# Performance work log

Measured on AMD Instinct MI355X. Metric: run time of the kernel, lower is better.

## Reference

```python
import jax, jax.numpy as jnp
import numpy as np

HEADS, OUT_C = 8, 16
NEG_SLOPE = 0.2  # PyG GATConv default negative_slope


def setup_inputs() -> dict:
    key = jax.random.key(0)
    ks = jax.random.split(key, 6)
    N, E, IN = 100000, 1600000, 128
    x = jax.random.normal(ks[0], (N, IN), jnp.float32)
    edge_index = jax.random.randint(ks[1], (2, E), 0, N, dtype=jnp.int32)
    W = jax.random.normal(ks[2], (IN, HEADS * OUT_C), jnp.float32) / np.float32(np.sqrt(IN))
    att_src = jax.random.normal(ks[3], (HEADS, OUT_C), jnp.float32) * 0.1
    att_dst = jax.random.normal(ks[4], (HEADS, OUT_C), jnp.float32) * 0.1
    bias = jax.random.normal(ks[5], (HEADS * OUT_C,), jnp.float32) * 0.01
    return {"x": x, "edge_index": edge_index, "W": W,
            "att_src": att_src, "att_dst": att_dst, "bias": bias}


def reference(x, edge_index, W, att_src, att_dst, bias):
    N = x.shape[0]
    # Linear projection, split into heads: [N, H, C]
    xw = (x @ W).reshape(N, HEADS, OUT_C)
    # Add self-loops (PyG default add_self_loops=True)
    loops = jnp.arange(N, dtype=edge_index.dtype)
    src = jnp.concatenate([edge_index[0], loops])
    dst = jnp.concatenate([edge_index[1], loops])
    # Per-node attention terms [N, H], then per-edge logits
    a_s = jnp.einsum('nhc,hc->nh', xw, att_src)
    a_d = jnp.einsum('nhc,hc->nh', xw, att_dst)
    e = a_s[src] + a_d[dst]                       # [Etot, H]
    e = jnp.where(e > 0, e, NEG_SLOPE * e)        # LeakyReLU
    # Segment softmax over edges grouped by destination node
    emax = jax.ops.segment_max(e, dst, num_segments=N)
    p = jnp.exp(e - emax[dst])
    denom = jax.ops.segment_sum(p, dst, num_segments=N)
    alpha = p / (denom[dst] + 1e-16)              # [Etot, H]
    # Weighted scatter-aggregate of source messages
    out = jax.ops.segment_sum(xw[src] * alpha[:, :, None], dst, num_segments=N)
    out = out.reshape(N, HEADS * OUT_C) + bias    # concat heads + bias
    return jax.nn.relu(out)                       # act='relu', norm=None
```

## Files before the change

kernel.cpp:

```cpp
#include <hip/hip_runtime.h>
#include <math.h>

#define HEADS 8
#define OUTC 16
#define HC 128
#define NEG_SLOPE 0.2f

#define BM 128
#define BK 32
#define XPAD 132
#define CAP 64
#define CHUNK 2048

typedef unsigned int uint;
typedef unsigned short ushort;

__device__ __forceinline__ ushort f2bf(float f) {
    uint u = __float_as_uint(f);
    u += 0x7FFFu + ((u >> 16) & 1u);
    return (ushort)(u >> 16);
}

__global__ __launch_bounds__(256, 4) void k_fused(
    const float* __restrict__ x, const float* __restrict__ W,
    const float* __restrict__ att_src, const float* __restrict__ att_dst,
    const int* __restrict__ ei,
    ushort* __restrict__ xwh, float* __restrict__ a_s, float* __restrict__ a_d,
    int* __restrict__ deg, int* __restrict__ csr,
    int N, int E, int SBLK) {
    __shared__ float xs[BK][XPAD];
    __shared__ float Ws[BK][XPAD];

    if (blockIdx.x < SBLK) {
        int b = blockIdx.x;
        int chunk = b >> 3;
        int r = b & 7;
        int R8 = (N + 7) >> 3;
        int lo = r * R8;
        int hi = lo + R8; if (hi > N) hi = N;

        int cbase = chunk * CHUNK;
        int srcs[8], dsts[8];
#pragma unroll
        for (int g = 0; g < 2; ++g) {
            int e = cbase + g * 1024 + 4 * (int)threadIdx.x;
            if (e + 3 < E) {
                int4 s4 = *(const int4*)&ei[e];
                int4 d4 = *(const int4*)&ei[E + e];
                srcs[4 * g + 0] = s4.x; srcs[4 * g + 1] = s4.y;
                srcs[4 * g + 2] = s4.z; srcs[4 * g + 3] = s4.w;
                dsts[4 * g + 0] = d4.x; dsts[4 * g + 1] = d4.y;
                dsts[4 * g + 2] = d4.z; dsts[4 * g + 3] = d4.w;
            } else {
#pragma unroll
                for (int j = 0; j < 4; ++j) {
                    int ee = e + j;
                    if (ee < E) {
                        srcs[4 * g + j] = ei[ee];
                        dsts[4 * g + j] = ei[E + ee];
                    } else {
                        dsts[4 * g + j] = -1;
                    }
                }
            }
        }
#pragma unroll
        for (int k = 0; k < 8; ++k) {
            int d = dsts[k];
            if (d >= lo && d < hi) {
                int slot = atomicAdd(&deg[d], 1);
                if (slot < CAP) csr[(size_t)d * CAP + slot] = srcs[k];
            }
        }
        return;
    }

    int t = threadIdx.x;
    int nb0 = (blockIdx.x - SBLK) * BM;
    int tc = t & 15;
    int tr = t >> 4;

    float acc[8][8];
#pragma unroll
    for (int i = 0; i < 8; ++i)
#pragma unroll
        for (int j = 0; j < 8; ++j) acc[i][j] = 0.0f;

    for (int k0 = 0; k0 < HC; k0 += BK) {
        int kk4 = (t & 7) * 4;
#pragma unroll
        for (int p = 0; p < 4; ++p) {
            int nr = (t >> 3) + p * 32;
            int node = nb0 + nr;
            float4 v = make_float4(0.f, 0.f, 0.f, 0.f);
            if (node < N) v = *(const float4*)&x[(size_t)node * HC + k0 + kk4];
            xs[kk4 + 0][nr] = v.x;
            xs[kk4 + 1][nr] = v.y;
            xs[kk4 + 2][nr] = v.z;
            xs[kk4 + 3][nr] = v.w;
        }
        int kk = t >> 3;
        int c4 = (t & 7) * 4;
#pragma unroll
        for (int j = 0; j < 4; ++j) {
            *(float4*)&Ws[kk][c4 + j * 32] =
                *(const float4*)&W[(size_t)(k0 + kk) * HC + c4 + j * 32];
        }
        __syncthreads();

#pragma unroll 4
        for (int k = 0; k < BK; ++k) {
            float xa[8], wa[8];
            *(float4*)&xa[0] = *(const float4*)&xs[k][tr * 8];
            *(float4*)&xa[4] = *(const float4*)&xs[k][tr * 8 + 4];
            *(float4*)&wa[0] = *(const float4*)&Ws[k][tc * 8];
            *(float4*)&wa[4] = *(const float4*)&Ws[k][tc * 8 + 4];
#pragma unroll
            for (int i = 0; i < 8; ++i)
#pragma unroll
                for (int j = 0; j < 8; ++j)
                    acc[i][j] = fmaf(xa[i], wa[j], acc[i][j]);
        }
        __syncthreads();
    }

    float as8[8], ad8[8];
#pragma unroll
    for (int j = 0; j < 8; ++j) {
        as8[j] = att_src[tc * 8 + j];
        ad8[j] = att_dst[tc * 8 + j];
    }
    int h = tc >> 1;
#pragma unroll
    for (int i = 0; i < 8; ++i) {
        int node = nb0 + tr * 8 + i;
        float vs = 0.f, vd = 0.f;
        ushort h8[8];
#pragma unroll
        for (int j = 0; j < 8; ++j) {
            vs = fmaf(acc[i][j], as8[j], vs);
            vd = fmaf(acc[i][j], ad8[j], vd);
            h8[j] = f2bf(acc[i][j]);
        }
        vs += __shfl_xor(vs, 1);
        vd += __shfl_xor(vd, 1);
        if (node < N) {
            *(uint4*)&xwh[(size_t)node * HC + tc * 8] = *(uint4*)&h8[0];
            if ((tc & 1) == 0) {
                a_s[node * HEADS + h] = vs;
                a_d[node * HEADS + h] = vd;
            }
        }
    }
}

__global__ __launch_bounds__(256) void k_node(
    const int* __restrict__ deg, const int* __restrict__ csr,
    const float* __restrict__ a_s, const float* __restrict__ a_d,
    const uint* __restrict__ xwh, const float* __restrict__ bias,
    float* __restrict__ out, int N) {
    int n = blockIdx.x * 4 + (threadIdx.x >> 6);
    if (n >= N) return;
    int l = threadIdx.x & 63;
    int hB = l >> 3;

    float asn = a_s[n * HEADS + hB];
    float adn = a_d[n * HEADS + hB];

    float v = asn + adn;
    v = v > 0.0f ? v : NEG_SLOPE * v;
    float p = __expf(v);
    float den = p;
    uint w = xwh[n * 64 + l];
    float acc0 = p * __uint_as_float(w << 16);
    float acc1 = p * __uint_as_float(w & 0xFFFF0000u);

    int cnt = deg[n];
    if (cnt > CAP) cnt = CAP;
    const int* row = csr + (size_t)n * CAP;
#pragma unroll 4
    for (int i = 0; i < cnt; ++i) {
        int s = row[i];
        float vv = a_s[s * HEADS + hB] + adn;
        vv = vv > 0.0f ? vv : NEG_SLOPE * vv;
        float pp = __expf(vv);
        den += pp;
        uint ww = xwh[s * 64 + l];
        acc0 = fmaf(pp, __uint_as_float(ww << 16), acc0);
        acc1 = fmaf(pp, __uint_as_float(ww & 0xFFFF0000u), acc1);
    }

    float inv = 1.0f / (den + 1e-16f);
    float2 b = *(const float2*)&bias[2 * l];
    float r0 = acc0 * inv + b.x;
    float r1 = acc1 * inv + b.y;
    float2 o;
    o.x = r0 > 0.0f ? r0 : 0.0f;
    o.y = r1 > 0.0f ? r1 : 0.0f;
    *(float2*)&out[(size_t)n * HC + 2 * l] = o;
}

extern "C" void kernel_launch(void* const* d_in, const int* in_sizes, int n_in,
                              void* d_out, int out_size, void* d_ws, size_t ws_size,
                              hipStream_t stream) {
    const float* x       = (const float*)d_in[0];
    const int*   ei      = (const int*)d_in[1];
    const float* W       = (const float*)d_in[2];
    const float* att_src = (const float*)d_in[3];
    const float* att_dst = (const float*)d_in[4];
    const float* bias    = (const float*)d_in[5];
    float* out = (float*)d_out;

    int N = in_sizes[0] / HC;
    int E = in_sizes[1] / 2;

    ushort* xwh = (ushort*)d_ws;
    float* a_s  = (float*)(xwh + (size_t)N * HC);
    float* a_d  = a_s + (size_t)N * HEADS;
    int* deg    = (int*)(a_d + (size_t)N * HEADS);
    int* csr    = deg + N;

    hipMemsetAsync(deg, 0, (size_t)N * sizeof(int), stream);

    int GB = (N + BM - 1) / BM;
    int SC = (E + CHUNK - 1) / CHUNK;
    int SBLK = SC * 8;
    k_fused<<<SBLK + GB, 256, 0, stream>>>(x, W, att_src, att_dst, ei,
                                           xwh, a_s, a_d, deg, csr, N, E, SBLK);

    k_node<<<(N + 3) / 4, 256, 0, stream>>>(deg, csr, a_s, a_d,
                                            (const uint*)xwh, bias, out, N);
}
```

Measured before the change: 310.8 us.

## Batch neighbor gathers, use exp2 with prescaled logits, reorder blocks, halve BK

```diff
diff --git a/kernel.cpp b/kernel.cpp
--- a/kernel.cpp
+++ b/kernel.cpp
@@ -5,15 +5,19 @@
 #define OUTC 16
 #define HC 128
 #define NEG_SLOPE 0.2f
+#define LOG2E 1.44269504f
 
 #define BM 128
-#define BK 32
+#define BK 16
 #define XPAD 132
 #define CAP 64
 #define CHUNK 2048
 
 typedef unsigned int uint;
 typedef unsigned short ushort;
+typedef float  __attribute__((ext_vector_type(4))) f32x4;
+typedef int    __attribute__((ext_vector_type(4))) i32x4;
+typedef uint   __attribute__((ext_vector_type(4))) u32x4;
 
 __device__ __forceinline__ ushort f2bf(float f) {
     uint u = __float_as_uint(f);
@@ -27,26 +31,28 @@
     const int* __restrict__ ei,
     ushort* __restrict__ xwh, float* __restrict__ a_s, float* __restrict__ a_d,
     int* __restrict__ deg, int* __restrict__ csr,
-    int N, int E, int SBLK) {
+    int N, int E, int GB) {
     __shared__ float xs[BK][XPAD];
     __shared__ float Ws[BK][XPAD];
 
-    if (blockIdx.x < SBLK) {
-        int b = blockIdx.x;
-        int chunk = b >> 3;
-        int r = b & 7;
+    int bid = blockIdx.x;
+    if (bid >= GB) {
+        int i = bid - GB;
+        int chunk = i >> 3;
+        int r = bid & 7;
         int R8 = (N + 7) >> 3;
         int lo = r * R8;
         int hi = lo + R8; if (hi > N) hi = N;
 
         int cbase = chunk * CHUNK;
+        int t = threadIdx.x;
         int srcs[8], dsts[8];
 #pragma unroll
         for (int g = 0; g < 2; ++g) {
-            int e = cbase + g * 1024 + 4 * (int)threadIdx.x;
+            int e = cbase + g * 1024 + 4 * t;
             if (e + 3 < E) {
-                int4 s4 = *(const int4*)&ei[e];
-                int4 d4 = *(const int4*)&ei[E + e];
+                i32x4 s4 = __builtin_nontemporal_load((const i32x4*)&ei[e]);
+                i32x4 d4 = __builtin_nontemporal_load((const i32x4*)&ei[E + e]);
                 srcs[4 * g + 0] = s4.x; srcs[4 * g + 1] = s4.y;
                 srcs[4 * g + 2] = s4.z; srcs[4 * g + 3] = s4.w;
                 dsts[4 * g + 0] = d4.x; dsts[4 * g + 1] = d4.y;
@@ -76,7 +82,7 @@
     }
 
     int t = threadIdx.x;
-    int nb0 = (blockIdx.x - SBLK) * BM;
+    int nb0 = bid * BM;
     int tc = t & 15;
     int tr = t >> 4;
 
@@ -86,25 +92,28 @@
 #pragma unroll
         for (int j = 0; j < 8; ++j) acc[i][j] = 0.0f;
 
+    int kk4 = (t & 3) * 4;
+    int xr  = t >> 2;
+    int wk  = t >> 4;
+    int wc4 = (t & 15) * 4;
+
     for (int k0 = 0; k0 < HC; k0 += BK) {
-        int kk4 = (t & 7) * 4;
-#pragma unroll
-        for (int p = 0; p < 4; ++p) {
-            int nr = (t >> 3) + p * 32;
+#pragma unroll
+        for (int p = 0; p < 2; ++p) {
+            int nr = xr + p * 64;
             int node = nb0 + nr;
-            float4 v = make_float4(0.f, 0.f, 0.f, 0.f);
-            if (node < N) v = *(const float4*)&x[(size_t)node * HC + k0 + kk4];
+            f32x4 v = {0.f, 0.f, 0.f, 0.f};
+            if (node < N)
+                v = __builtin_nontemporal_load((const f32x4*)&x[(size_t)node * HC + k0 + kk4]);
             xs[kk4 + 0][nr] = v.x;
             xs[kk4 + 1][nr] = v.y;
             xs[kk4 + 2][nr] = v.z;
             xs[kk4 + 3][nr] = v.w;
         }
-        int kk = t >> 3;
-        int c4 = (t & 7) * 4;
-#pragma unroll
-        for (int j = 0; j < 4; ++j) {
-            *(float4*)&Ws[kk][c4 + j * 32] =
-                *(const float4*)&W[(size_t)(k0 + kk) * HC + c4 + j * 32];
+#pragma unroll
+        for (int j = 0; j < 2; ++j) {
+            *(float4*)&Ws[wk][wc4 + j * 64] =
+                *(const float4*)&W[(size_t)(k0 + wk) * HC + wc4 + j * 64];
         }
         __syncthreads();
 
@@ -145,10 +154,11 @@
         vs += __shfl_xor(vs, 1);
         vd += __shfl_xor(vd, 1);
         if (node < N) {
-            *(uint4*)&xwh[(size_t)node * HC + tc * 8] = *(uint4*)&h8[0];
+            u32x4 hv = *(u32x4*)&h8[0];
+            __builtin_nontemporal_store(hv, (u32x4*)&xwh[(size_t)node * HC + tc * 8]);
             if ((tc & 1) == 0) {
-                a_s[node * HEADS + h] = vs;
-                a_d[node * HEADS + h] = vd;
+                a_s[node * HEADS + h] = vs * LOG2E;
+                a_d[node * HEADS + h] = vd * LOG2E;
             }
         }
     }
@@ -164,12 +174,11 @@
     int l = threadIdx.x & 63;
     int hB = l >> 3;
 
-    float asn = a_s[n * HEADS + hB];
     float adn = a_d[n * HEADS + hB];
 
-    float v = asn + adn;
+    float v = a_s[n * HEADS + hB] + adn;
     v = v > 0.0f ? v : NEG_SLOPE * v;
-    float p = __expf(v);
+    float p = exp2f(v);
     float den = p;
     uint w = xwh[n * 64 + l];
     float acc0 = p * __uint_as_float(w << 16);
@@ -178,16 +187,34 @@
     int cnt = deg[n];
     if (cnt > CAP) cnt = CAP;
     const int* row = csr + (size_t)n * CAP;
-#pragma unroll 4
-    for (int i = 0; i < cnt; ++i) {
-        int s = row[i];
-        float vv = a_s[s * HEADS + hB] + adn;
-        vv = vv > 0.0f ? vv : NEG_SLOPE * vv;
-        float pp = __expf(vv);
-        den += pp;
-        uint ww = xwh[s * 64 + l];
-        acc0 = fmaf(pp, __uint_as_float(ww << 16), acc0);
-        acc1 = fmaf(pp, __uint_as_float(ww & 0xFFFF0000u), acc1);
+
+    for (int base = 0; base < cnt; base += 8) {
+        int sv[8];
+#pragma unroll
+        for (int j = 0; j < 8; ++j) {
+            int i = base + j;
+            sv[j] = (i < cnt) ? row[i] : -1;
+        }
+        float as8[8];
+        uint w8[8];
+#pragma unroll
+        for (int j = 0; j < 8; ++j) {
+            if (sv[j] >= 0) {
+                as8[j] = a_s[sv[j] * HEADS + hB];
+                w8[j]  = xwh[(size_t)sv[j] * 64 + l];
+            }
+        }
+#pragma unroll
+        for (int j = 0; j < 8; ++j) {
+            if (sv[j] >= 0) {
+                float vv = as8[j] + adn;
+                vv = vv > 0.0f ? vv : NEG_SLOPE * vv;
+                float pp = exp2f(vv);
+                den += pp;
+                acc0 = fmaf(pp, __uint_as_float(w8[j] << 16), acc0);
+                acc1 = fmaf(pp, __uint_as_float(w8[j] & 0xFFFF0000u), acc1);
+            }
+        }
     }
 
     float inv = 1.0f / (den + 1e-16f);
@@ -225,8 +252,8 @@
     int GB = (N + BM - 1) / BM;
     int SC = (E + CHUNK - 1) / CHUNK;
     int SBLK = SC * 8;
-    k_fused<<<SBLK + GB, 256, 0, stream>>>(x, W, att_src, att_dst, ei,
-                                           xwh, a_s, a_d, deg, csr, N, E, SBLK);
+    k_fused<<<GB + SBLK, 256, 0, stream>>>(x, W, att_src, att_dst, ei,
+                                           xwh, a_s, a_d, deg, csr, N, E, GB);
 
     k_node<<<(N + 3) / 4, 256, 0, stream>>>(deg, csr, a_s, a_d,
                                             (const uint*)xwh, bias, out, N);
```

Measured after the change: 289.9 us. -6.7%, faster.
